# Performance work log

Hardware: AMD Instinct MI355X
Metric: run time of the kernel (lower is better)

## Reference

```python
import jax, jax.numpy as jnp
import numpy as np

N = 50000   # nodes
E = 800000  # edges
IN = 16     # in_channels
HID = 8     # hidden_channels (per-head)
H = 4       # heads
LAT = 32    # latent_dim
ED = 8      # edge_dim
D1 = H * HID      # 32  (conv1 output, concat)
D2 = H * D1       # 128 (middle conv output, concat)
NEG_SLOPE = 0.2


def setup_inputs() -> dict:
    key = jax.random.key(0)
    ks = jax.random.split(key, 24)
    g = lambda k, shape: jax.random.normal(k, shape, jnp.float32) * 0.1
    inp = {
        'x': jax.random.normal(ks[0], (N, IN), jnp.float32),
        'edge_index': jax.random.randint(ks[1], (2, E), 0, N, jnp.int32),
        'edge_attr': jax.random.normal(ks[2], (E, ED), jnp.float32),
        # conv1: in=16 -> heads=4, out=8 (concat -> 32)
        'Wl1': g(ks[3], (IN, D1)), 'bl1': jnp.zeros((D1,), jnp.float32),
        'Wr1': g(ks[4], (IN, D1)), 'br1': jnp.zeros((D1,), jnp.float32),
        'We1': g(ks[5], (ED, D1)), 'att1': g(ks[6], (H, HID)), 'b1': jnp.zeros((D1,), jnp.float32),
        # middle conv: in=32 -> heads=4, out=32 (concat -> 128), residual linear
        'Wl2': g(ks[7], (D1, D2)), 'bl2': jnp.zeros((D2,), jnp.float32),
        'Wr2': g(ks[8], (D1, D2)), 'br2': jnp.zeros((D2,), jnp.float32),
        'We2': g(ks[9], (ED, D2)), 'att2': g(ks[10], (H, D1)), 'b2': jnp.zeros((D2,), jnp.float32),
        'Rw2': g(ks[11], (D1, D2)),
        # conv_final: in=128 -> heads=1, out=32
        'Wl3': g(ks[12], (D2, LAT)), 'bl3': jnp.zeros((LAT,), jnp.float32),
        'Wr3': g(ks[13], (D2, LAT)), 'br3': jnp.zeros((LAT,), jnp.float32),
        'We3': g(ks[14], (ED, LAT)), 'att3': g(ks[15], (1, LAT)), 'b3': jnp.zeros((LAT,), jnp.float32),
    }
    return inp


def _segment_softmax(logits, seg, n):
    # logits: [E, H], seg: [E] target-node ids
    m = jax.lax.stop_gradient(jax.ops.segment_max(logits, seg, num_segments=n))
    e = jnp.exp(logits - m[seg])
    s = jax.ops.segment_sum(e, seg, num_segments=n)
    return e / s[seg]


def _gatv2_layer(x, src, dst, eattr, Wl, bl, Wr, br, We, att, bias, heads, out_ch, n, resW=None):
    # GATv2Conv (eval mode, concat=True): message = xl[src]*alpha,
    # alpha from LeakyReLU(xl[src] + xr[dst] + We@edge_attr) . att, edge-softmax over dst.
    xl = (x @ Wl + bl).reshape(n, heads, out_ch)
    xr = (x @ Wr + br).reshape(n, heads, out_ch)
    e = (eattr @ We).reshape(-1, heads, out_ch)
    m = xl[src] + xr[dst] + e                      # [E, H, C]
    s = jax.nn.leaky_relu(m, NEG_SLOPE)
    logits = jnp.einsum('ehc,hc->eh', s, att)      # [E, H]
    alpha = _segment_softmax(logits, dst, n)       # [E, H]
    out = jax.ops.segment_sum(alpha[:, :, None] * xl[src], dst, num_segments=n)
    out = out.reshape(n, heads * out_ch) + bias
    if resW is not None:
        out = out + x @ resW
    return out


def reference(x, edge_index, edge_attr, Wl1, bl1, Wr1, br1, We1, att1, b1,
              Wl2, bl2, Wr2, br2, We2, att2, b2, Rw2,
              Wl3, bl3, Wr3, br3, We3, att3, b3):
    src, dst = edge_index[0], edge_index[1]
    # add_self_loops with fill_value='mean': loop edge_attr = mean of incoming edge_attr
    ones = jnp.ones((src.shape[0],), x.dtype)
    deg = jax.ops.segment_sum(ones, dst, num_segments=N)
    loop_attr = jax.ops.segment_sum(edge_attr, dst, num_segments=N) / jnp.maximum(deg, 1.0)[:, None]
    loop = jnp.arange(N, dtype=src.dtype)
    s2 = jnp.concatenate([src, loop])
    d2 = jnp.concatenate([dst, loop])
    ea = jnp.concatenate([edge_attr, loop_attr], axis=0)

    h = jax.nn.relu(_gatv2_layer(x, s2, d2, ea, Wl1, bl1, Wr1, br1, We1, att1, b1, H, HID, N))
    h = jax.nn.relu(_gatv2_layer(h, s2, d2, ea, Wl2, bl2, Wr2, br2, We2, att2, b2, H, D1, N, resW=Rw2))
    out = _gatv2_layer(h, s2, d2, ea, Wl3, bl3, Wr3, br3, We3, att3, b3, 1, LAT, N)
    return out
```

## Files before the change

kernel.cpp:

```cpp
#include <hip/hip_runtime.h>
#include <hip/hip_fp16.h>

#define NEG_SLOPE 0.2f

constexpr int NN = 50000;
constexpr int EE = 800000;

static inline int cdiv(int a, int b) { return (a + b - 1) / b; }

typedef _Float16 h2 __attribute__((ext_vector_type(2)));

#if __has_builtin(__builtin_amdgcn_fdot2)
static __device__ inline float fdot2f(h2 a, h2 b, float c) {
    return __builtin_amdgcn_fdot2(a, b, c, false);
}
#else
static __device__ inline float fdot2f(h2 a, h2 b, float c) {
    return c + (float)a.x * (float)b.x + (float)a.y * (float)b.y;
}
#endif

static __device__ inline h2 bch2(unsigned u) { return __builtin_bit_cast(h2, u); }


__global__ void hist_kernel(const int4* __restrict__ dst4, int* __restrict__ rowcnt, int E4) {
    int t = blockIdx.x * blockDim.x + threadIdx.x;
    if (t >= E4) return;
    int4 d = dst4[t];
    atomicAdd(&rowcnt[d.x], 1);
    atomicAdd(&rowcnt[d.y], 1);
    atomicAdd(&rowcnt[d.z], 1);
    atomicAdd(&rowcnt[d.w], 1);
}

__global__ void scana_kernel(const int* __restrict__ cnt, int* __restrict__ blocksum, int n) {
    __shared__ int s[256];
    int t = threadIdx.x, g = blockIdx.x * 256 + t;
    s[t] = (g < n) ? cnt[g] + 1 : 0;
    __syncthreads();
    for (int off = 128; off > 0; off >>= 1) {
        if (t < off) s[t] += s[t + off];
        __syncthreads();
    }
    if (t == 0) blocksum[blockIdx.x] = s[0];
}

__global__ void scanb_kernel(const int* __restrict__ cnt, const int* __restrict__ blocksum,
                             int nbk, int* __restrict__ rowptr, int* __restrict__ cursor,
                             int* __restrict__ src_arr, int n) {
    __shared__ int bs[256];
    __shared__ int s[256];
    int t = threadIdx.x;
    bs[t] = (t < nbk) ? blocksum[t] : 0;
    __syncthreads();
    for (int off = 1; off < 256; off <<= 1) {
        int tv = (t >= off) ? bs[t - off] : 0; __syncthreads();
        bs[t] += tv; __syncthreads();
    }
    int blockoff = (blockIdx.x > 0) ? bs[blockIdx.x - 1] : 0;
    int g = blockIdx.x * 256 + t;
    int val = (g < n) ? cnt[g] + 1 : 0;
    s[t] = val; __syncthreads();
    for (int off = 1; off < 256; off <<= 1) {
        int tv = (t >= off) ? s[t - off] : 0; __syncthreads();
        s[t] += tv; __syncthreads();
    }
    if (g >= n) return;
    int incl = s[t] + blockoff;
    rowptr[g + 1] = incl;
    int beg = incl - val;
    cursor[g] = beg + 1;
    src_arr[beg] = g;
    if (g == 0) rowptr[0] = 0;
}

__global__ void scatter_kernel(const int* __restrict__ src, const int* __restrict__ dst,
                               const float* __restrict__ eattr,
                               int* __restrict__ cursor,
                               uint4* __restrict__ ea_arr, int* __restrict__ src_arr, int E) {
    int t = blockIdx.x * blockDim.x + threadIdx.x;
    if (t >= E) return;
    int d = dst[t];
    int pos = atomicAdd(&cursor[d], 1);
    const float4* ea4 = (const float4*)(eattr + (size_t)t * 8);
    float4 a = ea4[0], b = ea4[1];
    __half2 h0 = __floats2half2_rn(a.x, a.y);
    __half2 h1 = __floats2half2_rn(a.z, a.w);
    __half2 h2v = __floats2half2_rn(b.x, b.y);
    __half2 h3 = __floats2half2_rn(b.z, b.w);
    uint4 u;
    u.x = *(unsigned*)&h0; u.y = *(unsigned*)&h1;
    u.z = *(unsigned*)&h2v; u.w = *(unsigned*)&h3;
    ea_arr[pos] = u;
    src_arr[pos] = src[t];
}

template <int NB1>
__global__ __launch_bounds__(256) void fused_nl1_loopsea_kernel(
    const float* __restrict__ x,
    const float* __restrict__ Wl, const float* __restrict__ bl,
    const float* __restrict__ Wr, const float* __restrict__ br,
    __half* __restrict__ xl, __half* __restrict__ xr,
    const int* __restrict__ rowptr, uint4* __restrict__ ea_arr, int n) {
    constexpr int K = 16, CT = 32, NPB = 8;
    __shared__ float Wls[K * CT];
    __shared__ float Wrs[K * CT];
    __shared__ float xs[NPB * K];
    int tid = threadIdx.x;
    if (blockIdx.x < NB1) {
        int ty = tid >> 5, c = tid & 31;
        for (int i = tid; i < K * CT; i += 256) { Wls[i] = Wl[i]; Wrs[i] = Wr[i]; }
        int node0 = blockIdx.x * NPB;
        for (int i = tid; i < NPB * K; i += 256) {
            int nd = node0 + i / K;
            xs[i] = (nd < n) ? x[(size_t)node0 * K + i] : 0.f;
        }
        __syncthreads();
        int node = node0 + ty;
        if (node >= n) return;
        float aL = bl[c], aR = br[c];
        const float* xrow = &xs[ty * K];
        for (int k = 0; k < K; ++k) {
            float xv = xrow[k];
            aL = fmaf(xv, Wls[k * CT + c], aL);
            aR = fmaf(xv, Wrs[k * CT + c], aR);
        }
        xl[(size_t)node * CT + c] = __float2half(aL);
        xr[(size_t)node * CT + c] = __float2half(aR);
    } else {
        int wave = ((blockIdx.x - NB1) * 256 + tid) >> 6;
        int lane = tid & 63;
        if (wave >= n) return;
        int beg = rowptr[wave], end = rowptr[wave + 1];
        int k = lane & 7, j0 = lane >> 3;
        const __half* eap = (const __half*)ea_arr;
        float s = 0.f;
        for (int j = beg + 1 + j0; j < end; j += 8)
            s += __half2float(eap[(unsigned)j * 8 + k]);
        s += __shfl_xor(s, 8); s += __shfl_xor(s, 16); s += __shfl_xor(s, 32);
        int cnt = end - beg - 1;
        if (lane < 8) ((__half*)ea_arr)[(unsigned)beg * 8 + lane] =
            __float2half(s / fmaxf((float)cnt, 1.f));
    }
}

template <int K, int CT, int NPB>
__global__ __launch_bounds__(256) void node_linear_h_kernel(
    const __half* __restrict__ x,
    const float* __restrict__ Wl, const float* __restrict__ bl,
    const float* __restrict__ Wr, const float* __restrict__ br,
    __half* __restrict__ xl, __half* __restrict__ xr, int n) {
    constexpr int K2 = K / 2;
    constexpr int TS = 256 / CT;
    __shared__ h2 Wls[K2 * CT];
    __shared__ h2 Wrs[K2 * CT];
    __shared__ h2 xs[NPB * K2];
    int tid = threadIdx.x;
    for (int i = tid; i < K2 * CT; i += 256) {
        int k2 = i / CT, c = i % CT;
        Wls[i] = h2{(_Float16)Wl[(2 * k2) * CT + c], (_Float16)Wl[(2 * k2 + 1) * CT + c]};
        Wrs[i] = h2{(_Float16)Wr[(2 * k2) * CT + c], (_Float16)Wr[(2 * k2 + 1) * CT + c]};
    }
    int node0 = blockIdx.x * NPB;
    const unsigned* xg = (const unsigned*)(x + (size_t)node0 * K);
    for (int i = tid; i < NPB * K2; i += 256) {
        int nd = node0 + i / K2;
        unsigned u = (nd < n) ? xg[i] : 0u;
        xs[i] = bch2(u);
    }
    __syncthreads();
    int c = tid % CT, ty = tid / CT;
    int bound = (node0 + NPB < n) ? NPB : (n - node0);
    for (int local = ty; local < bound; local += TS) {
        int node = node0 + local;
        float aL = bl[c], aR = br[c];
        const h2* xrow = &xs[local * K2];
        for (int k = 0; k < K2; ++k) {
            h2 xv = xrow[k];
            aL = fdot2f(xv, Wls[k * CT + c], aL);
            aR = fdot2f(xv, Wrs[k * CT + c], aR);
        }
        xl[(size_t)node * CT + c] = __float2half(aL);
        xr[(size_t)node * CT + c] = __float2half(aR);
    }
}

template <int NPB>
__global__ __launch_bounds__(256) void nlh2_res_kernel(
    const __half* __restrict__ x,
    const float* __restrict__ Wl, const float* __restrict__ bl,
    const float* __restrict__ Wr, const float* __restrict__ br,
    const float* __restrict__ Rw,
    const float* __restrict__ b2,
    __half* __restrict__ xl, __half* __restrict__ xr,
    __half* __restrict__ res, int n) {
    constexpr int K = 32, CT = 128, K2 = K / 2;
    __shared__ h2 Wls[K2 * CT];
    __shared__ h2 Wrs[K2 * CT];
    __shared__ float Rws[K * CT];
    __shared__ h2 xs[NPB * K2];
    int tid = threadIdx.x;
    for (int i = tid; i < K2 * CT; i += 256) {
        int k2 = i / CT, c = i % CT;
        Wls[i] = h2{(_Float16)Wl[(2 * k2) * CT + c], (_Float16)Wl[(2 * k2 + 1) * CT + c]};
        Wrs[i] = h2{(_Float16)Wr[(2 * k2) * CT + c], (_Float16)Wr[(2 * k2 + 1) * CT + c]};
    }
    for (int i = tid; i < K * CT; i += 256) Rws[i] = Rw[i];
    int node0 = blockIdx.x * NPB;
    const unsigned* xg = (const unsigned*)(x + (size_t)node0 * K);
    for (int i = tid; i < NPB * K2; i += 256) {
        int nd = node0 + i / K2;
        unsigned u = (nd < n) ? xg[i] : 0u;
        xs[i] = bch2(u);
    }
    __syncthreads();
    int c = tid & 127, ty = tid >> 7;
    int bound = (node0 + NPB < n) ? NPB : (n - node0);
    for (int local = ty; local < bound; local += 2) {
        int node = node0 + local;
        float aL = bl[c], aR = br[c], aS = b2[c];
        const h2* xrow = &xs[local * K2];
        for (int k = 0; k < K2; ++k) {
            h2 xv = xrow[k];
            aL = fdot2f(xv, Wls[k * CT + c], aL);
            aR = fdot2f(xv, Wrs[k * CT + c], aR);
            aS = fmaf((float)xv.x, Rws[(2 * k) * CT + c], aS);
            aS = fmaf((float)xv.y, Rws[(2 * k + 1) * CT + c], aS);
        }
        xl[(size_t)node * CT + c] = __float2half(aL);
        xr[(size_t)node * CT + c] = __float2half(aR);
        res[(size_t)node * CT + c] = __float2half(aS);
    }
}

template <bool RELU, bool RES>
__global__ __launch_bounds__(256) void agg128_kernel(
    const int* __restrict__ rowptr,
    const uint4* __restrict__ ea_arr, const int* __restrict__ src_arr,
    const __half* __restrict__ xl, const __half* __restrict__ xr,
    const float* __restrict__ We,
    const float* __restrict__ att,
    const float* __restrict__ bias,
    __half* __restrict__ out, int n) {
    int tid = threadIdx.x;
    int node = (blockIdx.x * 256 + tid) >> 6;
    int lane = tid & 63;
    if (node >= n) return;
    int sub = lane >> 5, cl = lane & 31;
    int c0 = 4 * cl;
    h2 wch[4][4];
    float attc[4];
#pragma unroll
    for (int c = 0; c < 4; ++c) {
        attc[c] = att[c0 + c];
#pragma unroll
        for (int k = 0; k < 4; ++k)
            wch[c][k] = h2{(_Float16)We[(2 * k) * 128 + c0 + c],
                           (_Float16)We[(2 * k + 1) * 128 + c0 + c]};
    }
    int beg = rowptr[node], end = rowptr[node + 1];
    uint2 xru = *(const uint2*)&xr[(unsigned)(node * 128 + c0)];
    h2 xr01 = bch2(xru.x), xr23 = bch2(xru.y);
    float xrc[4] = {(float)xr01.x, (float)xr01.y, (float)xr23.x, (float)xr23.y};
    float num[4] = {0.f, 0.f, 0.f, 0.f};
    float den = 0.f;

    int j = beg + sub;
    uint4 u0, u1, u2; int s0, s1, s2; uint2 x0;
    if (j < end)     { u0 = ea_arr[j];     s0 = src_arr[j]; }
    if (j + 2 < end) { u1 = ea_arr[j + 2]; s1 = src_arr[j + 2]; }
    if (j + 4 < end) { u2 = ea_arr[j + 4]; s2 = src_arr[j + 4]; }
    if (j < end)     x0 = *(const uint2*)&xl[(unsigned)(s0 * 128 + c0)];
    while (j < end) {
        uint4 uT; int sT; uint2 xT;
        if (j + 6 < end) { uT = ea_arr[j + 6]; sT = src_arr[j + 6]; }
        if (j + 2 < end) { xT = *(const uint2*)&xl[(unsigned)(s1 * 128 + c0)]; }
        h2 e0 = bch2(u0.x), e1 = bch2(u0.y), e2 = bch2(u0.z), e3 = bch2(u0.w);
        h2 xl01 = bch2(x0.x), xl23 = bch2(x0.y);
        float xls[4] = {(float)xl01.x, (float)xl01.y, (float)xl23.x, (float)xl23.y};
        float p = 0.f;
#pragma unroll
        for (int c = 0; c < 4; ++c) {
            float m = xls[c] + xrc[c];
            m = fdot2f(e0, wch[c][0], m); m = fdot2f(e1, wch[c][1], m);
            m = fdot2f(e2, wch[c][2], m); m = fdot2f(e3, wch[c][3], m);
            float sv = fmaxf(m, 0.f) + NEG_SLOPE * fminf(m, 0.f);
            p = fmaf(sv, attc[c], p);
        }
        p += __shfl_xor(p, 1); p += __shfl_xor(p, 2); p += __shfl_xor(p, 4);
        float wgt = __expf(p);
#pragma unroll
        for (int c = 0; c < 4; ++c) num[c] = fmaf(wgt, xls[c], num[c]);
        den += wgt;
        j += 2;
        u0 = u1; u1 = u2; u2 = uT;
        s1 = s2; s2 = sT;
        x0 = xT;
    }
#pragma unroll
    for (int c = 0; c < 4; ++c) num[c] += __shfl_xor(num[c], 32);
    den += __shfl_xor(den, 32);
    if (sub == 0) {
        float inv = 1.f / den;
        float base[4];
        if (RES) {
            uint2 ru = *(const uint2*)&out[(unsigned)(node * 128 + c0)];
            h2 r01 = bch2(ru.x), r23 = bch2(ru.y);
            base[0] = (float)r01.x; base[1] = (float)r01.y;
            base[2] = (float)r23.x; base[3] = (float)r23.y;
        } else {
#pragma unroll
            for (int c = 0; c < 4; ++c) base[c] = bias[c0 + c];
        }
        float v[4];
#pragma unroll
        for (int c = 0; c < 4; ++c) v[c] = fmaf(num[c], inv, base[c]);
        if (RELU) {
#pragma unroll
            for (int c = 0; c < 4; ++c) v[c] = fmaxf(v[c], 0.f);
        }
        __half2 o01 = __floats2half2_rn(v[0], v[1]);
        __half2 o23 = __floats2half2_rn(v[2], v[3]);
        uint2 ou; ou.x = *(unsigned*)&o01; ou.y = *(unsigned*)&o23;
        *(uint2*)&out[(unsigned)(node * 128 + c0)] = ou;
    }
}

template <int HC, bool RELU, typename OUT>
__global__ __launch_bounds__(256) void agg32_kernel(
    const int* __restrict__ rowptr,
    const uint4* __restrict__ ea_arr, const int* __restrict__ src_arr,
    const __half* __restrict__ xl, const __half* __restrict__ xr,
    const float* __restrict__ We,
    const float* __restrict__ att,
    const float* __restrict__ bias,
    OUT* __restrict__ out, int n) {
    int tid = threadIdx.x;
    int node = (blockIdx.x * 256 + tid) >> 5;
    int lane = tid & 31;
    if (node >= n) return;
    int sub = lane >> 4, q = lane & 15;
    int c0 = 2 * q;
    h2 wc0[4], wc1[4];
#pragma unroll
    for (int k = 0; k < 4; ++k) {
        wc0[k] = h2{(_Float16)We[(2 * k) * 32 + c0], (_Float16)We[(2 * k + 1) * 32 + c0]};
        wc1[k] = h2{(_Float16)We[(2 * k) * 32 + c0 + 1], (_Float16)We[(2 * k + 1) * 32 + c0 + 1]};
    }
    float att0 = att[c0], att1 = att[c0 + 1];
    int beg = rowptr[node], end = rowptr[node + 1];
    h2 xrh = bch2(*(const unsigned*)&xr[(unsigned)(node * 32 + c0)]);
    float xrc0 = (float)xrh.x, xrc1 = (float)xrh.y;
    float num0 = 0.f, num1 = 0.f, den = 0.f;

    int j = beg + sub;
    uint4 u0, u1, u2; int s0, s1, s2; unsigned x0;
    if (j < end)     { u0 = ea_arr[j];     s0 = src_arr[j]; }
    if (j + 2 < end) { u1 = ea_arr[j + 2]; s1 = src_arr[j + 2]; }
    if (j + 4 < end) { u2 = ea_arr[j + 4]; s2 = src_arr[j + 4]; }
    if (j < end)     x0 = *(const unsigned*)&xl[(unsigned)(s0 * 32 + c0)];
    while (j < end) {
        uint4 uT; int sT; unsigned xT;
        if (j + 6 < end) { uT = ea_arr[j + 6]; sT = src_arr[j + 6]; }
        if (j + 2 < end) { xT = *(const unsigned*)&xl[(unsigned)(s1 * 32 + c0)]; }
        h2 e0 = bch2(u0.x), e1 = bch2(u0.y), e2 = bch2(u0.z), e3 = bch2(u0.w);
        h2 xlh = bch2(x0);
        float xls0 = (float)xlh.x, xls1 = (float)xlh.y;
        float m0 = xls0 + xrc0, m1 = xls1 + xrc1;
        m0 = fdot2f(e0, wc0[0], m0); m0 = fdot2f(e1, wc0[1], m0);
        m0 = fdot2f(e2, wc0[2], m0); m0 = fdot2f(e3, wc0[3], m0);
        m1 = fdot2f(e0, wc1[0], m1); m1 = fdot2f(e1, wc1[1], m1);
        m1 = fdot2f(e2, wc1[2], m1); m1 = fdot2f(e3, wc1[3], m1);
        float s0v = fmaxf(m0, 0.f) + NEG_SLOPE * fminf(m0, 0.f);
        float s1v = fmaxf(m1, 0.f) + NEG_SLOPE * fminf(m1, 0.f);
        float p = fmaf(s0v, att0, s1v * att1);
#pragma unroll
        for (int off = HC / 4; off > 0; off >>= 1) p += __shfl_xor(p, off);
        float wgt = __expf(p);
        num0 = fmaf(wgt, xls0, num0);
        num1 = fmaf(wgt, xls1, num1);
        den += wgt;
        j += 2;
        u0 = u1; u1 = u2; u2 = uT;
        s1 = s2; s2 = sT;
        x0 = xT;
    }
    num0 += __shfl_xor(num0, 16);
    num1 += __shfl_xor(num1, 16);
    den  += __shfl_xor(den, 16);
    if (sub == 0) {
        float inv = 1.f / den;
        float v0 = num0 * inv + bias[c0];
        float v1 = num1 * inv + bias[c0 + 1];
        if (RELU) { v0 = fmaxf(v0, 0.f); v1 = fmaxf(v1, 0.f); }
        if constexpr (sizeof(OUT) == 2) {
            __half2 o = __floats2half2_rn(v0, v1);
            *(__half2*)&out[(unsigned)(node * 32 + c0)] = o;
        } else {
            float2 o; o.x = v0; o.y = v1;
            *(float2*)&out[(size_t)node * 32 + c0] = o;
        }
    }
}

extern "C" void kernel_launch(void* const* d_in, const int* in_sizes, int n_in,
                              void* d_out, int out_size, void* d_ws, size_t ws_size,
                              hipStream_t stream) {
    const float* x    = (const float*)d_in[0];
    const int* ei     = (const int*)d_in[1];
    const float* eatt = (const float*)d_in[2];
    const float* Wl1 = (const float*)d_in[3],  *bl1 = (const float*)d_in[4];
    const float* Wr1 = (const float*)d_in[5],  *br1 = (const float*)d_in[6];
    const float* We1 = (const float*)d_in[7],  *att1 = (const float*)d_in[8];
    const float* b1  = (const float*)d_in[9];
    const float* Wl2 = (const float*)d_in[10], *bl2 = (const float*)d_in[11];
    const float* Wr2 = (const float*)d_in[12], *br2 = (const float*)d_in[13];
    const float* We2 = (const float*)d_in[14], *att2 = (const float*)d_in[15];
    const float* b2  = (const float*)d_in[16], *Rw2 = (const float*)d_in[17];
    const float* Wl3 = (const float*)d_in[18], *bl3 = (const float*)d_in[19];
    const float* Wr3 = (const float*)d_in[20], *br3 = (const float*)d_in[21];
    const float* We3 = (const float*)d_in[22], *att3 = (const float*)d_in[23];
    const float* b3  = (const float*)d_in[24];

    const int* srcp = ei;
    const int* dstp = ei + EE;

    char* w = (char*)d_ws;
    size_t off = 0;
    auto alloc = [&](size_t bytes) { char* p = w + off; off += (bytes + 255) & ~size_t(255); return p; };
    int*    rowcnt   = (int*)alloc((size_t)NN * 4);
    int*    rowptr   = (int*)alloc((size_t)(NN + 1) * 4);
    int*    cursor   = (int*)alloc((size_t)NN * 4);
    int*    blocksum = (int*)alloc(256 * 4);
    uint4*  ea_arr   = (uint4*)alloc((size_t)(EE + NN) * 16);
    int*    src_arr  = (int*)alloc((size_t)(EE + NN) * 4);
    __half* xlbuf    = (__half*)alloc((size_t)NN * 128 * 2);
    __half* xrbuf    = (__half*)alloc((size_t)NN * 128 * 2);
    __half* hA       = (__half*)alloc((size_t)NN * 32 * 2);
    __half* hB       = (__half*)alloc((size_t)NN * 128 * 2);

    int nb = cdiv(NN, 256);

    hipMemsetAsync(rowcnt, 0, (size_t)NN * 4, stream);
    hist_kernel<<<cdiv(EE / 4, 256), 256, 0, stream>>>((const int4*)dstp, rowcnt, EE / 4);
    scana_kernel<<<nb, 256, 0, stream>>>(rowcnt, blocksum, NN);
    scanb_kernel<<<nb, 256, 0, stream>>>(rowcnt, blocksum, nb, rowptr, cursor, src_arr, NN);
    scatter_kernel<<<cdiv(EE, 256), 256, 0, stream>>>(
        srcp, dstp, eatt, cursor, ea_arr, src_arr, EE);

    constexpr int NB1 = (NN + 7) / 8;
    int nb_ls = cdiv(NN, 4);
    fused_nl1_loopsea_kernel<NB1><<<NB1 + nb_ls, 256, 0, stream>>>(
        x, Wl1, bl1, Wr1, br1, xlbuf, xrbuf, rowptr, ea_arr, NN);

    agg32_kernel<8, true, __half><<<cdiv(NN, 8), 256, 0, stream>>>(
        rowptr, ea_arr, src_arr, xlbuf, xrbuf, We1, att1, b1, hA, NN);

    nlh2_res_kernel<32><<<cdiv(NN, 32), 256, 0, stream>>>(
        hA, Wl2, bl2, Wr2, br2, Rw2, b2, xlbuf, xrbuf, hB, NN);
    agg128_kernel<true, true><<<cdiv(NN, 4), 256, 0, stream>>>(
        rowptr, ea_arr, src_arr, xlbuf, xrbuf, We2, att2, b2, hB, NN);

    node_linear_h_kernel<128, 32, 64><<<cdiv(NN, 64), 256, 0, stream>>>(
        hB, Wl3, bl3, Wr3, br3, xlbuf, xrbuf, NN);
    agg32_kernel<32, false, float><<<cdiv(NN, 8), 256, 0, stream>>>(
        rowptr, ea_arr, src_arr, xlbuf, xrbuf, We3, att3, b3,
        (float*)d_out, NN);
}
```

Baseline: 404.9 us.

## Fuse self-loop edge-attr mean into first-layer aggregation kernel

Removes the separate pass that computed the mean incoming edge attribute for each node's self-loop slot. The first agg32 launch now accumulates the edge attributes while it walks the neighbours, writes the fp16 mean into the self-loop slot for later layers, and handles the self-loop term itself at the end. The node-linear part becomes its own small kernel. This saves one full read of the edge-attribute array, at the cost of extra registers and FP adds in the layer-1 aggregation.

```diff
diff --git a/kernel.cpp b/kernel.cpp
--- a/kernel.cpp
+++ b/kernel.cpp
@@ -95,53 +95,35 @@
     src_arr[pos] = src[t];
 }
 
-template <int NB1>
-__global__ __launch_bounds__(256) void fused_nl1_loopsea_kernel(
+__global__ __launch_bounds__(256) void nl1_kernel(
     const float* __restrict__ x,
     const float* __restrict__ Wl, const float* __restrict__ bl,
     const float* __restrict__ Wr, const float* __restrict__ br,
-    __half* __restrict__ xl, __half* __restrict__ xr,
-    const int* __restrict__ rowptr, uint4* __restrict__ ea_arr, int n) {
+    __half* __restrict__ xl, __half* __restrict__ xr, int n) {
     constexpr int K = 16, CT = 32, NPB = 8;
     __shared__ float Wls[K * CT];
     __shared__ float Wrs[K * CT];
     __shared__ float xs[NPB * K];
     int tid = threadIdx.x;
-    if (blockIdx.x < NB1) {
-        int ty = tid >> 5, c = tid & 31;
-        for (int i = tid; i < K * CT; i += 256) { Wls[i] = Wl[i]; Wrs[i] = Wr[i]; }
-        int node0 = blockIdx.x * NPB;
-        for (int i = tid; i < NPB * K; i += 256) {
-            int nd = node0 + i / K;
-            xs[i] = (nd < n) ? x[(size_t)node0 * K + i] : 0.f;
-        }
-        __syncthreads();
-        int node = node0 + ty;
-        if (node >= n) return;
-        float aL = bl[c], aR = br[c];
-        const float* xrow = &xs[ty * K];
-        for (int k = 0; k < K; ++k) {
-            float xv = xrow[k];
-            aL = fmaf(xv, Wls[k * CT + c], aL);
-            aR = fmaf(xv, Wrs[k * CT + c], aR);
-        }
-        xl[(size_t)node * CT + c] = __float2half(aL);
-        xr[(size_t)node * CT + c] = __float2half(aR);
-    } else {
-        int wave = ((blockIdx.x - NB1) * 256 + tid) >> 6;
-        int lane = tid & 63;
-        if (wave >= n) return;
-        int beg = rowptr[wave], end = rowptr[wave + 1];
-        int k = lane & 7, j0 = lane >> 3;
-        const __half* eap = (const __half*)ea_arr;
-        float s = 0.f;
-        for (int j = beg + 1 + j0; j < end; j += 8)
-            s += __half2float(eap[(unsigned)j * 8 + k]);
-        s += __shfl_xor(s, 8); s += __shfl_xor(s, 16); s += __shfl_xor(s, 32);
-        int cnt = end - beg - 1;
-        if (lane < 8) ((__half*)ea_arr)[(unsigned)beg * 8 + lane] =
-            __float2half(s / fmaxf((float)cnt, 1.f));
-    }
+    int ty = tid >> 5, c = tid & 31;
+    for (int i = tid; i < K * CT; i += 256) { Wls[i] = Wl[i]; Wrs[i] = Wr[i]; }
+    int node0 = blockIdx.x * NPB;
+    for (int i = tid; i < NPB * K; i += 256) {
+        int nd = node0 + i / K;
+        xs[i] = (nd < n) ? x[(size_t)node0 * K + i] : 0.f;
+    }
+    __syncthreads();
+    int node = node0 + ty;
+    if (node >= n) return;
+    float aL = bl[c], aR = br[c];
+    const float* xrow = &xs[ty * K];
+    for (int k = 0; k < K; ++k) {
+        float xv = xrow[k];
+        aL = fmaf(xv, Wls[k * CT + c], aL);
+        aR = fmaf(xv, Wrs[k * CT + c], aR);
+    }
+    xl[(size_t)node * CT + c] = __float2half(aL);
+    xr[(size_t)node * CT + c] = __float2half(aR);
 }
 
 template <int K, int CT, int NPB>
@@ -326,10 +308,10 @@
     }
 }
 
-template <int HC, bool RELU, typename OUT>
+template <int HC, bool SELF, bool RELU, typename OUT>
 __global__ __launch_bounds__(256) void agg32_kernel(
     const int* __restrict__ rowptr,
-    const uint4* __restrict__ ea_arr, const int* __restrict__ src_arr,
+    uint4* __restrict__ ea_arr, const int* __restrict__ src_arr,
     const __half* __restrict__ xl, const __half* __restrict__ xr,
     const float* __restrict__ We,
     const float* __restrict__ att,
@@ -352,8 +334,9 @@
     h2 xrh = bch2(*(const unsigned*)&xr[(unsigned)(node * 32 + c0)]);
     float xrc0 = (float)xrh.x, xrc1 = (float)xrh.y;
     float num0 = 0.f, num1 = 0.f, den = 0.f;
-
-    int j = beg + sub;
+    float easum[8] = {0.f, 0.f, 0.f, 0.f, 0.f, 0.f, 0.f, 0.f};
+
+    int j = beg + (SELF ? 1 : 0) + sub;
     uint4 u0, u1, u2; int s0, s1, s2; unsigned x0;
     if (j < end)     { u0 = ea_arr[j];     s0 = src_arr[j]; }
     if (j + 2 < end) { u1 = ea_arr[j + 2]; s1 = src_arr[j + 2]; }
@@ -364,6 +347,12 @@
         if (j + 6 < end) { uT = ea_arr[j + 6]; sT = src_arr[j + 6]; }
         if (j + 2 < end) { xT = *(const unsigned*)&xl[(unsigned)(s1 * 32 + c0)]; }
         h2 e0 = bch2(u0.x), e1 = bch2(u0.y), e2 = bch2(u0.z), e3 = bch2(u0.w);
+        if (SELF) {
+            easum[0] += (float)e0.x; easum[1] += (float)e0.y;
+            easum[2] += (float)e1.x; easum[3] += (float)e1.y;
+            easum[4] += (float)e2.x; easum[5] += (float)e2.y;
+            easum[6] += (float)e3.x; easum[7] += (float)e3.y;
+        }
         h2 xlh = bch2(x0);
         float xls0 = (float)xlh.x, xls1 = (float)xlh.y;
         float m0 = xls0 + xrc0, m1 = xls1 + xrc1;
@@ -384,6 +373,41 @@
         u0 = u1; u1 = u2; u2 = uT;
         s1 = s2; s2 = sT;
         x0 = xT;
+    }
+    if (SELF) {
+#pragma unroll
+        for (int c = 0; c < 8; ++c) easum[c] += __shfl_xor(easum[c], 16);
+        float invc = 1.f / fmaxf((float)(end - beg - 1), 1.f);
+        h2 mh0 = h2{(_Float16)(easum[0] * invc), (_Float16)(easum[1] * invc)};
+        h2 mh1 = h2{(_Float16)(easum[2] * invc), (_Float16)(easum[3] * invc)};
+        h2 mh2 = h2{(_Float16)(easum[4] * invc), (_Float16)(easum[5] * invc)};
+        h2 mh3 = h2{(_Float16)(easum[6] * invc), (_Float16)(easum[7] * invc)};
+        if (lane == 0) {
+            uint4 mu;
+            mu.x = __builtin_bit_cast(unsigned, mh0);
+            mu.y = __builtin_bit_cast(unsigned, mh1);
+            mu.z = __builtin_bit_cast(unsigned, mh2);
+            mu.w = __builtin_bit_cast(unsigned, mh3);
+            ea_arr[beg] = mu;
+        }
+        h2 xlh = bch2(*(const unsigned*)&xl[(unsigned)(node * 32 + c0)]);
+        float xls0 = (float)xlh.x, xls1 = (float)xlh.y;
+        float m0 = xls0 + xrc0, m1 = xls1 + xrc1;
+        m0 = fdot2f(mh0, wc0[0], m0); m0 = fdot2f(mh1, wc0[1], m0);
+        m0 = fdot2f(mh2, wc0[2], m0); m0 = fdot2f(mh3, wc0[3], m0);
+        m1 = fdot2f(mh0, wc1[0], m1); m1 = fdot2f(mh1, wc1[1], m1);
+        m1 = fdot2f(mh2, wc1[2], m1); m1 = fdot2f(mh3, wc1[3], m1);
+        float s0v = fmaxf(m0, 0.f) + NEG_SLOPE * fminf(m0, 0.f);
+        float s1v = fmaxf(m1, 0.f) + NEG_SLOPE * fminf(m1, 0.f);
+        float p = fmaf(s0v, att0, s1v * att1);
+#pragma unroll
+        for (int off = HC / 4; off > 0; off >>= 1) p += __shfl_xor(p, off);
+        float wgt = __expf(p);
+        if (sub == 0) {
+            num0 = fmaf(wgt, xls0, num0);
+            num1 = fmaf(wgt, xls1, num1);
+            den += wgt;
+        }
     }
     num0 += __shfl_xor(num0, 16);
     num1 += __shfl_xor(num1, 16);
@@ -448,12 +472,10 @@
     scatter_kernel<<<cdiv(EE, 256), 256, 0, stream>>>(
         srcp, dstp, eatt, cursor, ea_arr, src_arr, EE);
 
-    constexpr int NB1 = (NN + 7) / 8;
-    int nb_ls = cdiv(NN, 4);
-    fused_nl1_loopsea_kernel<NB1><<<NB1 + nb_ls, 256, 0, stream>>>(
-        x, Wl1, bl1, Wr1, br1, xlbuf, xrbuf, rowptr, ea_arr, NN);
-
-    agg32_kernel<8, true, __half><<<cdiv(NN, 8), 256, 0, stream>>>(
+    nl1_kernel<<<cdiv(NN, 8), 256, 0, stream>>>(
+        x, Wl1, bl1, Wr1, br1, xlbuf, xrbuf, NN);
+
+    agg32_kernel<8, true, true, __half><<<cdiv(NN, 8), 256, 0, stream>>>(
         rowptr, ea_arr, src_arr, xlbuf, xrbuf, We1, att1, b1, hA, NN);
 
     nlh2_res_kernel<32><<<cdiv(NN, 32), 256, 0, stream>>>(
@@ -463,7 +485,7 @@
 
     node_linear_h_kernel<128, 32, 64><<<cdiv(NN, 64), 256, 0, stream>>>(
         hB, Wl3, bl3, Wr3, br3, xlbuf, xrbuf, NN);
-    agg32_kernel<32, false, float><<<cdiv(NN, 8), 256, 0, stream>>>(
+    agg32_kernel<32, false, false, float><<<cdiv(NN, 8), 256, 0, stream>>>(
         rowptr, ea_arr, src_arr, xlbuf, xrbuf, We3, att3, b3,
         (float*)d_out, NN);
 }
```

Measured after the change: 402.0 us. About the same (-0.7%).
